# Kernel tuning notes

Measured on AMD Instinct MI355X. Metric: run time of the kernel, lower is better.

Reference implementation:

```python
import jax, jax.numpy as jnp
import numpy as np
import math

B, L, D = 2, 2048, 1024
H, T, F = 16, 4, 4096
DK = D // H
EPS = 1e-5


def setup_inputs() -> dict:
    key = jax.random.key(0)
    ks = jax.random.split(key, 20)
    s = 0.02
    inp = {
        "x": jax.random.normal(ks[0], (B, L, D), jnp.float32),
        "token_types": jax.random.randint(ks[1], (B, L), 0, 4, jnp.int32),
        "seq_lens": jax.random.randint(ks[2], (B,), L // 2, L + 1, jnp.int32),
        "Wq": jax.random.normal(ks[3], (D, D), jnp.float32) * s,
        "Wk": jax.random.normal(ks[4], (D, D), jnp.float32) * s,
        "Wv": jax.random.normal(ks[5], (D, D), jnp.float32) * s,
        "Wu": jax.random.normal(ks[6], (D, D), jnp.float32) * s,
        "Wo": jax.random.normal(ks[7], (D, D), jnp.float32) * s,
        "ln1_g": jnp.ones((T, D), jnp.float32),
        "ln1_b": jnp.zeros((T, D), jnp.float32),
        "W1": jax.random.normal(ks[8], (T, D, F), jnp.float32) * s,
        "b1": jnp.zeros((T, F), jnp.float32),
        "W2": jax.random.normal(ks[9], (T, F, D), jnp.float32) * s,
        "b2": jnp.zeros((T, D), jnp.float32),
        "ln2_g": jnp.ones((T, D), jnp.float32),
        "ln2_b": jnp.zeros((T, D), jnp.float32),
    }
    return inp


def _token_ln(x, g, b, token_types):
    # normalization is identical across types; only gamma/beta differ per type
    mu = jnp.mean(x, axis=-1, keepdims=True)
    var = jnp.mean(jnp.square(x - mu), axis=-1, keepdims=True)
    xn = (x - mu) / jnp.sqrt(var + EPS)
    return xn * g[token_types] + b[token_types]


def _hstu_attn(x, token_types, seq_lens, Wq, Wk, Wv, Wu, Wo):
    neg = jnp.finfo(x.dtype).min
    Q = (x @ Wq).reshape(B, L, H, DK)
    K = (x @ Wk).reshape(B, L, H, DK)
    V = (x @ Wv).reshape(B, L, H, DK)
    U = (x @ Wu).reshape(B, L, H, DK)
    scores = jnp.einsum('blhd,bmhd->bhlm', Q, K) / math.sqrt(DK)  # [B,H,L,L]
    # hybrid mask: allow j<=i (causal) OR key j is a prompt token (type<3)
    is_prompt_j = (token_types < 3)[:, None, :]                    # [B,1,L]
    causal_ok = jnp.tril(jnp.ones((L, L), bool))[None]             # [1,L,L]
    allow = causal_ok | is_prompt_j                                 # [B,L,L]
    scores = scores + jnp.where(allow, 0.0, neg)[:, None]
    # padding mask on keys
    pad = jnp.arange(L)[None, :] >= seq_lens[:, None]               # [B,L]
    scores = jnp.where(pad[:, None, None, :], neg, scores)
    attn = jax.nn.softmax(scores, axis=-1)
    out = jnp.einsum('bhlm,bmhd->blhd', attn, V) * U                # U-gating
    return out.reshape(B, L, D) @ Wo


def _token_ffn(x, token_types, W1, b1, W2, b2):
    out = jnp.zeros_like(x)
    for t in range(T):  # fixed small number of token types
        h = jax.nn.gelu(x @ W1[t] + b1[t], approximate=False) @ W2[t] + b2[t]
        out = out + jnp.where((token_types == t)[..., None], h, 0.0)
    return out


def reference(x, token_types, seq_lens, Wq, Wk, Wv, Wu, Wo,
              ln1_g, ln1_b, W1, b1, W2, b2, ln2_g, ln2_b):
    h = _hstu_attn(x, token_types, seq_lens, Wq, Wk, Wv, Wu, Wo)
    x = _token_ln(x + h, ln1_g, ln1_b, token_types)
    h = _token_ffn(x, token_types, W1, b1, W2, b2)
    x = _token_ln(x + h, ln2_g, ln2_b, token_types)
    return x
```

## Files before the change

### kernel.cpp

```cpp
#include <hip/hip_runtime.h>
#include <hip/hip_bf16.h>
#include <math.h>

#define B_   2
#define L_   2048
#define D_   1024
#define H_   16
#define DK_  64
#define T_   4
#define F_   4096
#define NTOK (B_ * L_)

typedef __bf16 bf16_t;
typedef bf16_t bf16x8 __attribute__((ext_vector_type(8)));
typedef float  f32x4  __attribute__((ext_vector_type(4)));
typedef unsigned short u16;
typedef u16 u16x8 __attribute__((ext_vector_type(8)));
typedef unsigned long long ull;

static __device__ __forceinline__ u16 f2b(float f) {
    __hip_bfloat16 h = __float2bfloat16(f);
    return *reinterpret_cast<u16*>(&h);
}
static __device__ __forceinline__ float b2f(u16 u) {
    __hip_bfloat16 h;
    *reinterpret_cast<u16*>(&h) = u;
    return __bfloat162float(h);
}

static __device__ __forceinline__ void gld16(void* lds, const void* g) {
    __builtin_amdgcn_global_load_lds(
        (const __attribute__((address_space(1))) unsigned int*)g,
        (__attribute__((address_space(3))) unsigned int*)lds,
        16, 0, 0);
}

#define VMW(N) do { asm volatile("s_waitcnt vmcnt(" #N ")" ::: "memory"); \
                    __builtin_amdgcn_sched_barrier(0); } while (0)
#define BARR() do { __builtin_amdgcn_sched_barrier(0); \
                    __builtin_amdgcn_s_barrier();      \
                    __builtin_amdgcn_sched_barrier(0); } while (0)

__global__ void k_cast_bf16(const float* __restrict__ in, u16* __restrict__ out, int n4) {
    int i = blockIdx.x * 256 + threadIdx.x;
    if (i >= n4) return;
    float4 v = reinterpret_cast<const float4*>(in)[i];
    ushort4 o;
    o.x = f2b(v.x); o.y = f2b(v.y); o.z = f2b(v.z); o.w = f2b(v.w);
    reinterpret_cast<ushort4*>(out)[i] = o;
}

__global__ void k_tcast(const float* __restrict__ W, u16* __restrict__ Wt,
                        int K, int N, long sW, long sWt) {
    __shared__ float tile[32][65];
    int z = blockIdx.z;
    W  += (long)z * sW;
    Wt += (long)z * sWt;
    int n0 = blockIdx.x * 32, k0 = blockIdx.y * 64;
    int tx = threadIdx.x, ty = threadIdx.y;
#pragma unroll
    for (int i = 0; i < 8; i++)
        tile[tx][ty + 8 * i] = W[(long)(k0 + ty + 8 * i) * N + n0 + tx];
    __syncthreads();
#pragma unroll
    for (int i = 0; i < 4; i++) {
        int n = ty + 8 * i;
        unsigned lo = f2b(tile[n][2 * tx]);
        unsigned hi = f2b(tile[n][2 * tx + 1]);
        reinterpret_cast<unsigned*>(Wt)[(((long)(n0 + n) * K + k0) >> 1) + tx] = lo | (hi << 16);
    }
}

__global__ void k_tcast5(const float* __restrict__ Wq, const float* __restrict__ Wk,
                         const float* __restrict__ Wv, const float* __restrict__ Wu,
                         const float* __restrict__ Wo, u16* __restrict__ WT,
                         u16* __restrict__ WOT) {
    __shared__ float tile[32][65];
    int z = blockIdx.z;
    const float* W;
    u16* Wt;
    if      (z == 0) { W = Wq; Wt = WT; }
    else if (z == 1) { W = Wk; Wt = WT + 1048576; }
    else if (z == 2) { W = Wv; Wt = WT + 2097152; }
    else if (z == 3) { W = Wu; Wt = WT + 3145728; }
    else             { W = Wo; Wt = WOT; }
    int n0 = blockIdx.x * 32, k0 = blockIdx.y * 64;
    int tx = threadIdx.x, ty = threadIdx.y;
#pragma unroll
    for (int i = 0; i < 8; i++)
        tile[tx][ty + 8 * i] = W[(long)(k0 + ty + 8 * i) * 1024 + n0 + tx];
    __syncthreads();
#pragma unroll
    for (int i = 0; i < 4; i++) {
        int n = ty + 8 * i;
        unsigned lo = f2b(tile[n][2 * tx]);
        unsigned hi = f2b(tile[n][2 * tx + 1]);
        reinterpret_cast<unsigned*>(Wt)[(((long)(n0 + n) * 1024 + k0) >> 1) + tx] = lo | (hi << 16);
    }
}

enum { EP_BF16 = 0, EP_F32 = 1, EP_GELU_BF16 = 2, EP_BIAS_F32 = 3 };

template <int MODE, bool AIDX, bool CIDX, bool GROUPED, bool VTOUT>
__global__ __launch_bounds__(256, 2)
void k_g2(const u16* __restrict__ A, const u16* __restrict__ Bt,
          void* __restrict__ Cv, u16* __restrict__ VTbuf,
          const float* __restrict__ bias,
          const int* __restrict__ idxb, const int* __restrict__ boff,
          const int* __restrict__ bcnt,
          int M, int K, int lda, int ldb, int ldc,
          long strideB, int biasStride)
{
    const int gx = gridDim.x;
    const int nwg = gx * gridDim.y;
    const int id = blockIdx.y * gx + blockIdx.x;
    const int q8 = nwg >> 3, r8 = nwg & 7, xcd = id & 7, sub = id >> 3;
    const int id2 = (xcd < r8 ? xcd * (q8 + 1) : r8 * (q8 + 1) + (xcd - r8) * q8) + sub;
    const int tm = id2 % gx, tn = id2 / gx;
    const int bm = tm * 128, bn = tn * 128;

    int pend = M;
    if (GROUPED) {
        bool dead = true;
        int g = 0;
#pragma unroll
        for (int t = 0; t < T_; t++) {
            int o = boff[t], c = bcnt[t];
            int pe = o + (((c + 127) >> 7) << 7);
            if (bm >= o && bm < pe) { g = t; pend = o + c; dead = false; }
        }
        if (dead) return;
        Bt += (long)g * strideB;
        bias += (long)g * biasStride;
    }

    const int tid = threadIdx.x;
    const int wid = tid >> 6, lane = tid & 63;
    const int lg = lane >> 4, lr = lane & 15;
    const int wr = wid >> 1, wc = wid & 1;

    __shared__ u16 lds[4 * 8192];

    const u16* gA[4];
    const u16* gB[4];
#pragma unroll
    for (int i = 0; i < 4; i++) {
        int s = tid + 256 * i;
        int row = s >> 3;
        int sch = (s & 7) ^ (row & 7);
        int pa = bm + row;
        if (GROUPED) pa = min(pa, pend - 1);
        long ra = AIDX ? (long)idxb[pa] : (long)pa;
        gA[i] = A + ra * lda + sch * 8;
        gB[i] = Bt + (long)(bn + row) * ldb + sch * 8;
    }
    auto STAGE = [&](u16* bufp, long ko) {
#pragma unroll
        for (int i = 0; i < 4; i++)
            gld16(bufp + (tid + 256 * i) * 8, gA[i] + ko);
#pragma unroll
        for (int i = 0; i < 4; i++)
            gld16(bufp + 8192 + (tid + 256 * i) * 8, gB[i] + ko);
    };

    int cko[2];
#pragma unroll
    for (int kk = 0; kk < 2; kk++) cko[kk] = ((4 * kk + lg) ^ (lr & 7)) * 8;
    int offA[4], offB[4];
#pragma unroll
    for (int i = 0; i < 4; i++) {
        offA[i] = (wr * 64 + i * 16 + lr) * 64;
        offB[i] = (wc * 64 + i * 16 + lr) * 64;
    }

    const f32x4 zero = {0.f, 0.f, 0.f, 0.f};
    f32x4 acc[4][4];
#pragma unroll
    for (int m = 0; m < 4; m++)
#pragma unroll
        for (int n = 0; n < 4; n++) acc[m][n] = zero;

    const int NT = K >> 6;

    STAGE(lds, 0);

    for (int t = 0; t < NT; t++) {
        u16* bb_ = lds + (t & 1) * 16384;
        u16* bnx = lds + ((t & 1) ^ 1) * 16384;
        if (t + 1 < NT) {
            STAGE(bnx, (long)(t + 1) * 64);
            VMW(8);
        } else {
            VMW(0);
        }
        BARR();

        bf16x8 av[4][2], bv[4][2];
#pragma unroll
        for (int i = 0; i < 4; i++)
#pragma unroll
            for (int kk = 0; kk < 2; kk++) {
                av[i][kk] = *reinterpret_cast<const bf16x8*>(bb_ + offA[i] + cko[kk]);
                bv[i][kk] = *reinterpret_cast<const bf16x8*>(bb_ + 8192 + offB[i] + cko[kk]);
            }
        __builtin_amdgcn_s_setprio(1);
#pragma unroll
        for (int kk = 0; kk < 2; kk++)
#pragma unroll
            for (int m = 0; m < 4; m++)
#pragma unroll
                for (int n = 0; n < 4; n++)
                    acc[m][n] = __builtin_amdgcn_mfma_f32_16x16x32_bf16(
                        av[m][kk], bv[n][kk], acc[m][n], 0, 0, 0);
        __builtin_amdgcn_s_setprio(0);
        BARR();
    }

    if (VTOUT && bn >= 2048 && bn < 3072) {
#pragma unroll
        for (int m = 0; m < 4; m++) {
            int tok0 = bm + wr * 64 + m * 16 + lg * 4;
            int bb2 = tok0 >> 11, tin = tok0 & 2047;
#pragma unroll
            for (int n = 0; n < 4; n++) {
                int gn = bn + wc * 64 + n * 16 + lr;
                int d = gn - 2048, hh = d >> 6, dk = d & 63;
                ushort4 o4;
                o4.x = f2b(acc[m][n][0]); o4.y = f2b(acc[m][n][1]);
                o4.z = f2b(acc[m][n][2]); o4.w = f2b(acc[m][n][3]);
                long vi = ((long)(bb2 * 16 + hh) * 64 + dk) * 2048 + tin;
                *reinterpret_cast<ushort4*>(VTbuf + vi) = o4;
            }
        }
        return;
    }
#pragma unroll
    for (int m = 0; m < 4; m++) {
#pragma unroll
        for (int r = 0; r < 4; r++) {
            int prow = bm + wr * 64 + m * 16 + lg * 4 + r;
            if (GROUPED && prow >= pend) continue;
            long crow = CIDX ? (long)idxb[prow] : (long)prow;
#pragma unroll
            for (int n = 0; n < 4; n++) {
                int gn = bn + wc * 64 + n * 16 + lr;
                float v = acc[m][n][r];
                long off = crow * (long)ldc + gn;
                if (MODE == EP_GELU_BF16) {
                    v += bias[gn];
                    v = 0.5f * v * (1.0f + erff(v * 0.70710678118654752f));
                }
                if (MODE == EP_BIAS_F32) v += bias[gn];
                if (MODE == EP_BF16 || MODE == EP_GELU_BF16)
                    ((u16*)Cv)[off] = f2b(v);
                else
                    ((float*)Cv)[off] = v;
            }
        }
    }
}

#define KVB 128
__global__ __launch_bounds__(256)
void k_attn(const u16* __restrict__ cat, const u16* __restrict__ VT,
            const int* __restrict__ types, const int* __restrict__ seql,
            u16* __restrict__ AG)
{
    const int qt = blockIdx.x, h = blockIdx.y, b = blockIdx.z;
    const int tid = threadIdx.x, w = tid >> 6, lane = tid & 63;
    const int lg = lane >> 4, lr = lane & 15;
    const int qbase = qt * 64;

    __shared__ u16 sK[KVB * 64];
    __shared__ u16 sV[64 * KVB];
    __shared__ u16 sP[4 * 16 * KVB];
    __shared__ ull smask[4];

    const int seqlen = seql[b];
    const float QSC = 0.125f * 1.44269504f;
    const u16* vtb = VT + (long)(b * 16 + h) * 64 * 2048;

    const long qrow = (long)(b * L_ + qbase + w * 16 + lr);
    const u16* qp = cat + qrow * 4096 + h * 64;
    bf16x8 qf0, qf1, onesv;
    {
        u16x8 a0 = *reinterpret_cast<const u16x8*>(qp + lg * 8);
        u16x8 a1 = *reinterpret_cast<const u16x8*>(qp + 32 + lg * 8);
#pragma unroll
        for (int e = 0; e < 8; e++) {
            qf0[e] = (bf16_t)(b2f(a0[e]) * QSC);
            qf1[e] = (bf16_t)(b2f(a1[e]) * QSC);
            onesv[e] = (bf16_t)1.0f;
        }
    }

    const f32x4 zero = {0.f, 0.f, 0.f, 0.f};
    f32x4 o[4] = {zero, zero, zero, zero};
    f32x4 lsum4 = zero;
    float mrow[4] = {-1e30f, -1e30f, -1e30f, -1e30f};

    for (int kb = 0; kb < L_; kb += KVB) {
        if (kb >= seqlen) break;
#pragma unroll
        for (int i = 0; i < 4; i++) {
            int c = tid + 256 * i;
            int row = c >> 3, sl = (c & 7) ^ (row & 7);
            gld16(sK + c * 8, cat + (long)(b * L_ + kb + row) * 4096 + 1024 + h * 64 + sl * 8);
        }
#pragma unroll
        for (int i = 0; i < 4; i++) {
            int c = tid + 256 * i;
            int row = c >> 4, ch = c & 15;
            int sl = ch ^ (row & 15);
            gld16(sV + c * 8, vtb + (long)row * 2048 + kb + sl * 8);
        }
        if (w < 2) {
            int j = kb + w * 64 + lane;
            ull pm = __ballot(j >= seqlen);
            ull rm = __ballot(types[b * L_ + j] < 3);
            if (lane == 0) { smask[w * 2] = pm; smask[w * 2 + 1] = rm; }
        }
        __syncthreads();
        const ull pad0 = smask[0], pr0 = smask[1], pad1 = smask[2], pr1 = smask[3];

        f32x4 s[8];
#pragma unroll
        for (int n = 0; n < 8; n++) {
            int row = n * 16 + lr, r7 = row & 7;
            bf16x8 bk0 = *reinterpret_cast<const bf16x8*>(sK + row * 64 + ((lg ^ r7)) * 8);
            bf16x8 bk1 = *reinterpret_cast<const bf16x8*>(sK + row * 64 + (((lg ^ 4)) ^ r7) * 8);
            f32x4 t4 = zero;
            t4 = __builtin_amdgcn_mfma_f32_16x16x32_bf16(qf0, bk0, t4, 0, 0, 0);
            t4 = __builtin_amdgcn_mfma_f32_16x16x32_bf16(qf1, bk1, t4, 0, 0, 0);
            s[n] = t4;
        }

        float tmax[4] = {-1e30f, -1e30f, -1e30f, -1e30f};
        const bool interior = (kb + KVB <= qbase) && (kb + KVB <= seqlen);
        const bool future   = (kb > qbase + 63);
        if (interior) {
#pragma unroll
            for (int n = 0; n < 8; n++)
#pragma unroll
                for (int r = 0; r < 4; r++) tmax[r] = fmaxf(tmax[r], s[n][r]);
        } else if (future) {
            const ull d0 = pad0 | ~pr0, d1 = pad1 | ~pr1;
#pragma unroll
            for (int n = 0; n < 8; n++) {
                bool dead = (((n < 4) ? d0 : d1) >> (((n & 3) * 16 + lr))) & 1ull;
#pragma unroll
                for (int r = 0; r < 4; r++) {
                    float sv = dead ? -1e30f : s[n][r];
                    s[n][r] = sv;
                    tmax[r] = fmaxf(tmax[r], sv);
                }
            }
        } else {
            ull dm0[4], dm1[4];
#pragma unroll
            for (int r = 0; r < 4; r++) {
                int d = qbase + w * 16 + 4 * lg + r - kb;
                ull h0 = (d < 0) ? ~0ull : ((d >= 63) ? 0ull : (~0ull << (d + 1)));
                ull h1 = (d < 64) ? ~0ull : ((d >= 127) ? 0ull : (~0ull << (d - 63)));
                dm0[r] = pad0 | (~pr0 & h0);
                dm1[r] = pad1 | (~pr1 & h1);
            }
#pragma unroll
            for (int n = 0; n < 8; n++) {
                int bp = (n & 3) * 16 + lr;
#pragma unroll
                for (int r = 0; r < 4; r++) {
                    bool dead = (((n < 4) ? dm0[r] : dm1[r]) >> bp) & 1ull;
                    float sv = dead ? -1e30f : s[n][r];
                    s[n][r] = sv;
                    tmax[r] = fmaxf(tmax[r], sv);
                }
            }
        }
        bool grew = (tmax[0] > mrow[0]) || (tmax[1] > mrow[1]) ||
                    (tmax[2] > mrow[2]) || (tmax[3] > mrow[3]);
        if (__any(grew)) {
#pragma unroll
            for (int r = 0; r < 4; r++) {
#pragma unroll
                for (int d = 1; d < 16; d <<= 1)
                    tmax[r] = fmaxf(tmax[r], __shfl_xor(tmax[r], d, 64));
            }
            float corr[4];
#pragma unroll
            for (int r = 0; r < 4; r++) {
                float mnew = fmaxf(mrow[r], tmax[r]);
                corr[r] = __builtin_amdgcn_exp2f(mrow[r] - mnew);
                mrow[r] = mnew;
                lsum4[r] *= corr[r];
            }
#pragma unroll
            for (int n2 = 0; n2 < 4; n2++) {
                f32x4 t4 = o[n2];
#pragma unroll
                for (int r = 0; r < 4; r++) t4[r] *= corr[r];
                o[n2] = t4;
            }
        }
#pragma unroll
        for (int n = 0; n < 8; n++)
#pragma unroll
            for (int r = 0; r < 4; r++)
                s[n][r] = __builtin_amdgcn_exp2f(s[n][r] - mrow[r]);
        u16* Pw = sP + w * (16 * KVB);
#pragma unroll
        for (int n = 0; n < 8; n++) {
            int pc = n * 2 + (lr >> 3), p7 = lr & 7;
#pragma unroll
            for (int r = 0; r < 4; r++) {
                int q = 4 * lg + r;
                Pw[q * KVB + (pc ^ q) * 8 + p7] = f2b(s[n][r]);
            }
        }
        bf16x8 pa[4];
#pragma unroll
        for (int st = 0; st < 4; st++)
            pa[st] = *reinterpret_cast<const bf16x8*>(Pw + lr * KVB + ((st * 4 + lg) ^ lr) * 8);
#pragma unroll
        for (int st = 0; st < 4; st++)
            lsum4 = __builtin_amdgcn_mfma_f32_16x16x32_bf16(pa[st], onesv, lsum4, 0, 0, 0);
#pragma unroll
        for (int n2 = 0; n2 < 4; n2++) {
            int row = n2 * 16 + lr, r15 = row & 15;
            f32x4 t4 = o[n2];
#pragma unroll
            for (int st = 0; st < 4; st++) {
                bf16x8 vb = *reinterpret_cast<const bf16x8*>(sV + row * KVB + ((st * 4 + lg) ^ r15) * 8);
                t4 = __builtin_amdgcn_mfma_f32_16x16x32_bf16(pa[st], vb, t4, 0, 0, 0);
            }
            o[n2] = t4;
        }
        __syncthreads();
    }
#pragma unroll
    for (int n2 = 0; n2 < 4; n2++) {
#pragma unroll
        for (int r = 0; r < 4; r++) {
            int ig = qbase + w * 16 + 4 * lg + r;
            long orow = (long)(b * L_ + ig);
            int j = n2 * 16 + lr;
            float u = b2f(cat[orow * 4096 + 3072 + h * 64 + j]);
            float val = o[n2][r] / lsum4[r] * u;
            AG[orow * 1024 + h * 64 + j] = f2b(val);
        }
    }
}

template <bool WB>
__global__ __launch_bounds__(256)
void k_ln(const float* __restrict__ xa, const float* __restrict__ ha,
          const float* __restrict__ g, const float* __restrict__ bb,
          const int* __restrict__ types,
          float* __restrict__ of, u16* __restrict__ ob)
{
    const int tok = blockIdx.x, tid = threadIdx.x;
    const long base = (long)tok * D_;
    float4 va = reinterpret_cast<const float4*>(xa + base)[tid];
    float4 vh = reinterpret_cast<const float4*>(ha + base)[tid];
    float v0 = va.x + vh.x, v1 = va.y + vh.y, v2 = va.z + vh.z, v3 = va.w + vh.w;
    float s = v0 + v1 + v2 + v3;
    float ss = v0 * v0 + v1 * v1 + v2 * v2 + v3 * v3;
#pragma unroll
    for (int d = 1; d < 64; d <<= 1) { s += __shfl_xor(s, d, 64); ss += __shfl_xor(ss, d, 64); }
    __shared__ float red[8];
    if ((tid & 63) == 0) { red[tid >> 6] = s; red[4 + (tid >> 6)] = ss; }
    __syncthreads();
    s  = red[0] + red[1] + red[2] + red[3];
    ss = red[4] + red[5] + red[6] + red[7];
    const float mu  = s * (1.f / D_);
    const float var = ss * (1.f / D_) - mu * mu;
    const float inv = rsqrtf(var + 1e-5f);
    const int t = types[tok];
    const float* gp = g + (long)t * D_ + tid * 4;
    const float* bp = bb + (long)t * D_ + tid * 4;
    float o0 = (v0 - mu) * inv * gp[0] + bp[0];
    float o1 = (v1 - mu) * inv * gp[1] + bp[1];
    float o2 = (v2 - mu) * inv * gp[2] + bp[2];
    float o3 = (v3 - mu) * inv * gp[3] + bp[3];
    reinterpret_cast<float4*>(of + base)[tid] = make_float4(o0, o1, o2, o3);
    if (WB) {
        ushort4 u4;
        u4.x = f2b(o0); u4.y = f2b(o1); u4.z = f2b(o2); u4.w = f2b(o3);
        reinterpret_cast<ushort4*>(ob + base)[tid] = u4;
    }
}

__global__ void k_bucket(const int* __restrict__ types, int* __restrict__ cnt,
                         int* __restrict__ off, int* __restrict__ idxb) {
    __shared__ int lc[4], lo[4], lcur[4];
    const int tid = threadIdx.x;
    if (tid < 4) lc[tid] = 0;
    __syncthreads();
    int ty[4];
#pragma unroll
    for (int i = 0; i < 4; i++) {
        ty[i] = types[tid + 1024 * i];
        atomicAdd(&lc[ty[i]], 1);
    }
    __syncthreads();
    if (tid == 0) {
        int a = 0;
        for (int t = 0; t < T_; t++) {
            lo[t] = a; lcur[t] = 0;
            a += ((lc[t] + 127) >> 7) << 7;
        }
    }
    __syncthreads();
#pragma unroll
    for (int i = 0; i < 4; i++) {
        int p = atomicAdd(&lcur[ty[i]], 1);
        idxb[lo[ty[i]] + p] = tid + 1024 * i;
    }
    if (tid < 4) { cnt[tid] = lc[tid]; off[tid] = lo[tid]; }
}

extern "C" void kernel_launch(void* const* d_in, const int* in_sizes, int n_in,
                              void* d_out, int out_size, void* d_ws, size_t ws_size,
                              hipStream_t stream) {
    const float* x    = (const float*)d_in[0];
    const int* types  = (const int*)d_in[1];
    const int* seql   = (const int*)d_in[2];
    const float* Wq   = (const float*)d_in[3];
    const float* Wk   = (const float*)d_in[4];
    const float* Wv   = (const float*)d_in[5];
    const float* Wu   = (const float*)d_in[6];
    const float* Wo   = (const float*)d_in[7];
    const float* ln1g = (const float*)d_in[8];
    const float* ln1b = (const float*)d_in[9];
    const float* W1   = (const float*)d_in[10];
    const float* b1   = (const float*)d_in[11];
    const float* W2   = (const float*)d_in[12];
    const float* b2   = (const float*)d_in[13];
    const float* ln2g = (const float*)d_in[14];
    const float* ln2b = (const float*)d_in[15];

    char* ws = (char*)d_ws;
    constexpr size_t OFF_WT  = 0;
    constexpr size_t OFF_WOT = OFF_WT  + (size_t)4096 * 1024 * 2;
    constexpr size_t OFF_W1T = OFF_WOT + (size_t)1024 * 1024 * 2;
    constexpr size_t OFF_W2T = OFF_W1T + (size_t)T_ * 4096 * 1024 * 2;
    constexpr size_t OFF_XB  = OFF_W2T + (size_t)T_ * 4096 * 1024 * 2;
    constexpr size_t OFF_CAT = OFF_XB  + (size_t)NTOK * D_ * 2;
    constexpr size_t OFF_H   = OFF_CAT + (size_t)(NTOK + 512) * 4096 * 2;
    constexpr size_t OFF_X1  = OFF_H   + (size_t)NTOK * D_ * 4;
    constexpr size_t OFF_X1B = OFF_X1  + (size_t)NTOK * D_ * 4;
    constexpr size_t OFF_INT = OFF_X1B + (size_t)NTOK * D_ * 2;

    u16* WT   = (u16*)(ws + OFF_WT);
    u16* WOT  = (u16*)(ws + OFF_WOT);
    u16* W1T  = (u16*)(ws + OFF_W1T);
    u16* W2T  = (u16*)(ws + OFF_W2T);
    u16* XB   = (u16*)(ws + OFF_XB);
    u16* CAT  = (u16*)(ws + OFF_CAT);
    float* Hb = (float*)(ws + OFF_H);
    u16* VT   = (u16*)(ws + OFF_H);
    float* X1 = (float*)(ws + OFF_X1);
    u16* X1B  = (u16*)(ws + OFF_X1B);
    int* ibase = (int*)(ws + OFF_INT);
    int* cnt = ibase, *off = ibase + 4, *idxb = ibase + 8;

    dim3 blk(256), tb(32, 8);
    const int MT_PAD = 36;

    k_cast_bf16<<<NTOK * D_ / 4 / 256, blk, 0, stream>>>(x, XB, NTOK * D_ / 4);
    k_tcast5<<<dim3(32, 16, 5), tb, 0, stream>>>(Wq, Wk, Wv, Wu, Wo, WT, WOT);
    k_tcast<<<dim3(128, 16, T_), tb, 0, stream>>>(W1, W1T, 1024, 4096, (long)1024 * 4096, (long)4096 * 1024);
    k_tcast<<<dim3(32, 64, T_), tb, 0, stream>>>(W2, W2T, 4096, 1024, (long)4096 * 1024, (long)1024 * 4096);

    k_g2<EP_BF16, false, false, false, true><<<dim3(32, 32), blk, 0, stream>>>(
        XB, WT, CAT, VT, nullptr, nullptr, nullptr, nullptr,
        NTOK, 1024, 1024, 1024, 4096, 0, 0);

    k_attn<<<dim3(L_ / 64, H_, B_), blk, 0, stream>>>(CAT, VT, types, seql, XB);

    k_g2<EP_F32, false, false, false, false><<<dim3(32, 8), blk, 0, stream>>>(
        XB, WOT, Hb, nullptr, nullptr, nullptr, nullptr, nullptr,
        NTOK, 1024, 1024, 1024, 1024, 0, 0);

    k_ln<true><<<NTOK, blk, 0, stream>>>(x, Hb, ln1g, ln1b, types, X1, X1B);

    k_bucket<<<1, 1024, 0, stream>>>(types, cnt, off, idxb);

    k_g2<EP_GELU_BF16, true, false, true, false><<<dim3(MT_PAD, 32), blk, 0, stream>>>(
        X1B, W1T, CAT, nullptr, b1, idxb, off, cnt,
        NTOK, 1024, 1024, 1024, 4096, (long)4096 * 1024, 4096);

    k_g2<EP_BIAS_F32, false, true, true, false><<<dim3(MT_PAD, 8), blk, 0, stream>>>(
        CAT, W2T, Hb, nullptr, b2, idxb, off, cnt,
        NTOK, 4096, 4096, 4096, 1024, (long)1024 * 4096, 1024);

    k_ln<false><<<NTOK, blk, 0, stream>>>(X1, Hb, ln2g, ln2b, types, (float*)d_out, nullptr);
}
```

Measured before the change: 388.7 us.

## Prefetch next K/V tile into registers during attention compute

Replaces the synchronous global-to-LDS K/V loads in the attention loop with a register-staged software pipeline. The next tile's K and V are loaded into registers before the current tile's MFMA work and written to LDS after it, with the mask ballots, so global memory latency overlaps compute. The cost is 8 extra 16-byte vector registers per thread, which may lower occupancy, plus an extra barrier per iteration. The loop bound is now precomputed from seqlen.

After: 440.7 us. 1.13x slower.

```diff
diff --git a/kernel.cpp b/kernel.cpp
--- a/kernel.cpp
+++ b/kernel.cpp
@@ -280,6 +280,50 @@
     const float QSC = 0.125f * 1.44269504f;
     const u16* vtb = VT + (long)(b * 16 + h) * 64 * 2048;
 
+    const u16* gK[4];
+    const u16* gV[4];
+    int dstK[4], dstV[4];
+#pragma unroll
+    for (int i = 0; i < 4; i++) {
+        int c = tid + 256 * i;
+        int rowK = c >> 3, slK = (c & 7) ^ (rowK & 7);
+        gK[i] = cat + (long)(b * L_ + rowK) * 4096 + 1024 + h * 64 + slK * 8;
+        dstK[i] = c * 8;
+        int rowV = c >> 4, chV = c & 15, slV = chV ^ (rowV & 15);
+        gV[i] = vtb + (long)rowV * 2048 + slV * 8;
+        dstV[i] = c * 8;
+    }
+    u16x8 rk0, rk1, rk2, rk3, rv0, rv1, rv2, rv3;
+#define LOADKV(KB) do {                                                        \
+    long koK = (long)(KB) * 4096, koV = (KB);                                  \
+    rk0 = *reinterpret_cast<const u16x8*>(gK[0] + koK);                        \
+    rk1 = *reinterpret_cast<const u16x8*>(gK[1] + koK);                        \
+    rk2 = *reinterpret_cast<const u16x8*>(gK[2] + koK);                        \
+    rk3 = *reinterpret_cast<const u16x8*>(gK[3] + koK);                        \
+    rv0 = *reinterpret_cast<const u16x8*>(gV[0] + koV);                        \
+    rv1 = *reinterpret_cast<const u16x8*>(gV[1] + koV);                        \
+    rv2 = *reinterpret_cast<const u16x8*>(gV[2] + koV);                        \
+    rv3 = *reinterpret_cast<const u16x8*>(gV[3] + koV);                        \
+} while (0)
+#define WRITEKV() do {                                                         \
+    *reinterpret_cast<u16x8*>(sK + dstK[0]) = rk0;                             \
+    *reinterpret_cast<u16x8*>(sK + dstK[1]) = rk1;                             \
+    *reinterpret_cast<u16x8*>(sK + dstK[2]) = rk2;                             \
+    *reinterpret_cast<u16x8*>(sK + dstK[3]) = rk3;                             \
+    *reinterpret_cast<u16x8*>(sV + dstV[0]) = rv0;                             \
+    *reinterpret_cast<u16x8*>(sV + dstV[1]) = rv1;                             \
+    *reinterpret_cast<u16x8*>(sV + dstV[2]) = rv2;                             \
+    *reinterpret_cast<u16x8*>(sV + dstV[3]) = rv3;                             \
+} while (0)
+#define BALLOTS(KB) do {                                                       \
+    if (w < 2) {                                                               \
+        int j = (KB) + w * 64 + lane;                                          \
+        ull pm = __ballot(j >= seqlen);                                        \
+        ull rm = __ballot(types[b * L_ + j] < 3);                              \
+        if (lane == 0) { smask[w * 2] = pm; smask[w * 2 + 1] = rm; }           \
+    }                                                                          \
+} while (0)
+
     const long qrow = (long)(b * L_ + qbase + w * 16 + lr);
     const u16* qp = cat + qrow * 4096 + h * 64;
     bf16x8 qf0, qf1, onesv;
@@ -299,28 +343,20 @@
     f32x4 lsum4 = zero;
     float mrow[4] = {-1e30f, -1e30f, -1e30f, -1e30f};
 
-    for (int kb = 0; kb < L_; kb += KVB) {
-        if (kb >= seqlen) break;
-#pragma unroll
-        for (int i = 0; i < 4; i++) {
-            int c = tid + 256 * i;
-            int row = c >> 3, sl = (c & 7) ^ (row & 7);
-            gld16(sK + c * 8, cat + (long)(b * L_ + kb + row) * 4096 + 1024 + h * 64 + sl * 8);
-        }
-#pragma unroll
-        for (int i = 0; i < 4; i++) {
-            int c = tid + 256 * i;
-            int row = c >> 4, ch = c & 15;
-            int sl = ch ^ (row & 15);
-            gld16(sV + c * 8, vtb + (long)row * 2048 + kb + sl * 8);
-        }
-        if (w < 2) {
-            int j = kb + w * 64 + lane;
-            ull pm = __ballot(j >= seqlen);
-            ull rm = __ballot(types[b * L_ + j] < 3);
-            if (lane == 0) { smask[w * 2] = pm; smask[w * 2 + 1] = rm; }
-        }
-        __syncthreads();
+    const int nt = (seqlen + KVB - 1) / KVB;
+
+    LOADKV(0);
+    WRITEKV();
+    BALLOTS(0);
+    __syncthreads();
+
+    for (int ti = 0; ti < nt; ti++) {
+        const int kb = ti * KVB;
+        const bool s1 = (ti + 1 < nt);
+        if (s1) {
+            LOADKV(kb + KVB);
+            __builtin_amdgcn_sched_barrier(0);
+        }
         const ull pad0 = smask[0], pr0 = smask[1], pad1 = smask[2], pr1 = smask[3];
 
         f32x4 s[8];
@@ -436,6 +472,11 @@
             o[n2] = t4;
         }
         __syncthreads();
+        if (s1) {
+            WRITEKV();
+            BALLOTS(kb + KVB);
+            __syncthreads();
+        }
     }
 #pragma unroll
     for (int n2 = 0; n2 < 4; n2++) {
@@ -449,6 +490,9 @@
             AG[orow * 1024 + h * 64 + j] = f2b(val);
         }
     }
+#undef LOADKV
+#undef WRITEKV
+#undef BALLOTS
 }
 
 template <bool WB>
```
